# Kernel optimization log

Hardware: AMD Instinct MI355X
Metric: run time of the kernel (lower is better)

Reference implementation:

```python
import jax, jax.numpy as jnp
import numpy as np

N_NODES = 100000
N_EDGES = 1280000
D_IN = 64
D_HID = 64
D_OUT = 1
N_GRAPHS = 512


def setup_inputs() -> dict:
    key = jax.random.key(0)
    ks = jax.random.split(key, 12)
    x = jax.random.normal(ks[0], (N_NODES, D_IN), dtype=jnp.float32)
    edge_index = jax.random.randint(ks[1], (2, N_EDGES), 0, N_NODES, dtype=jnp.int32)
    batch = jnp.sort(jax.random.randint(ks[2], (N_NODES,), 0, N_GRAPHS, dtype=jnp.int32))
    s = 0.1
    w0 = jax.random.normal(ks[3], (D_IN, D_HID), dtype=jnp.float32) * s
    b0 = jnp.zeros((D_HID,), dtype=jnp.float32)
    w1 = jax.random.normal(ks[4], (D_HID, D_HID), dtype=jnp.float32) * s
    b1 = jnp.zeros((D_HID,), dtype=jnp.float32)
    w2 = jax.random.normal(ks[5], (D_HID, D_HID), dtype=jnp.float32) * s
    b2 = jnp.zeros((D_HID,), dtype=jnp.float32)
    fc_w = jax.random.normal(ks[6], (D_HID, D_OUT), dtype=jnp.float32) * s
    fc_b = jnp.zeros((D_OUT,), dtype=jnp.float32)
    return {"x": x, "edge_index": edge_index, "batch": batch,
            "w0": w0, "b0": b0, "w1": w1, "b1": b1, "w2": w2, "b2": b2,
            "fc_w": fc_w, "fc_b": fc_b}


def _gcn_conv(x, w, b, src, dst):
    # PyG GCNConv: h = x @ W; out_i = sum_j norm_ij * h_j over (A + I), sym norm.
    h = x @ w                                           # [N, H]
    ones = jnp.ones((src.shape[0],), dtype=h.dtype)
    deg = jax.ops.segment_sum(ones, dst, num_segments=N_NODES) + 1.0  # +1 self-loop
    dinv = jax.lax.rsqrt(deg)                           # [N]
    norm = dinv[src] * dinv[dst]                        # [E]
    agg = jax.ops.segment_sum(h[src] * norm[:, None], dst, num_segments=N_NODES)
    agg = agg + h * (dinv * dinv)[:, None]              # self-loop term
    return agg + b


def reference(x, edge_index, batch, w0, b0, w1, b1, w2, b2, fc_w, fc_b):
    src, dst = edge_index[0], edge_index[1]
    # 3 stacked GCNConv + relu (dropout is identity in eval mode)
    h = jax.nn.relu(_gcn_conv(x, w0, b0, src, dst))
    h = jax.nn.relu(_gcn_conv(h, w1, b1, src, dst))
    h = jax.nn.relu(_gcn_conv(h, w2, b2, src, dst))
    # global mean pool per graph
    sums = jax.ops.segment_sum(h, batch, num_segments=N_GRAPHS)        # [G, H]
    cnt = jax.ops.segment_sum(jnp.ones((N_NODES,), h.dtype), batch, num_segments=N_GRAPHS)
    mean = sums / jnp.maximum(cnt, 1.0)[:, None]
    return mean @ fc_w + fc_b                            # [G, 1]
```

## Files before the change

kernel.cpp:

```cpp
#include <hip/hip_runtime.h>
#include <hip/hip_fp16.h>
#include <type_traits>

#define N_NODES 100000
#define N_EDGES 1280000
#define N_GRAPHS 512
#define NBK 196
#define CHUNK 3200
#define NCH 400
#define CAP 8192
#define NDCAP 48
#define GEMM_BLOCKS 391

typedef _Float16 v8h __attribute__((ext_vector_type(8)));
typedef float v4f __attribute__((ext_vector_type(4)));

__device__ inline void fmix_lo(float& acc, unsigned h2, float n) {
    asm volatile("v_fma_mix_f32 %0, %1, %2, %0 op_sel:[0,0,0] op_sel_hi:[1,0,0]"
                 : "+v"(acc) : "v"(h2), "v"(n));
}
__device__ inline void fmix_hi(float& acc, unsigned h2, float n) {
    asm volatile("v_fma_mix_f32 %0, %1, %2, %0 op_sel:[1,0,0] op_sel_hi:[1,0,0]"
                 : "+v"(acc) : "v"(h2), "v"(n));
}


template <typename T, bool FOLD>
__device__ inline void gemm_body(int bid, const T* __restrict__ X,
                                 const float* __restrict__ W,
                                 const float* __restrict__ dinv,
                                 __half* __restrict__ H,
                                 _Float16 (*Wt)[72]) {
    int t = threadIdx.x;
    #pragma unroll
    for (int q = 0; q < 4; q++) {
        int idx = t + q * 256;
        int k = idx >> 4;
        int n0 = (idx & 15) * 4;
        float4 v = ((const float4*)W)[idx];
        Wt[n0 + 0][k] = (_Float16)v.x;
        Wt[n0 + 1][k] = (_Float16)v.y;
        Wt[n0 + 2][k] = (_Float16)v.z;
        Wt[n0 + 3][k] = (_Float16)v.w;
    }
    __syncthreads();

    int wv = t >> 6, lane = t & 63;
    int m = lane & 15, quad = lane >> 4;

    v8h bf[4][2];
    #pragma unroll
    for (int c = 0; c < 4; c++)
        #pragma unroll
        for (int h = 0; h < 2; h++)
            bf[c][h] = *(const v8h*)&Wt[c * 16 + m][h * 32 + quad * 8];

    int base = bid * 256 + wv * 64;
    #pragma unroll
    for (int tt = 0; tt < 4; tt++) {
        int tile = base + tt * 16;
        int rA = min(tile + m, N_NODES - 1);
        v8h a0, a1;
        if constexpr (std::is_same<T, float>::value) {
            const float* xp = (const float*)X + (size_t)rA * 64 + quad * 8;
            float4 p0 = *(const float4*)xp;
            float4 p1 = *(const float4*)(xp + 4);
            float4 p2 = *(const float4*)(xp + 32);
            float4 p3 = *(const float4*)(xp + 36);
            a0 = (v8h){(_Float16)p0.x, (_Float16)p0.y, (_Float16)p0.z, (_Float16)p0.w,
                       (_Float16)p1.x, (_Float16)p1.y, (_Float16)p1.z, (_Float16)p1.w};
            a1 = (v8h){(_Float16)p2.x, (_Float16)p2.y, (_Float16)p2.z, (_Float16)p2.w,
                       (_Float16)p3.x, (_Float16)p3.y, (_Float16)p3.z, (_Float16)p3.w};
        } else {
            const _Float16* xp = (const _Float16*)X + (size_t)rA * 64 + quad * 8;
            a0 = *(const v8h*)xp;
            a1 = *(const v8h*)(xp + 32);
        }
        v4f acc[4];
        #pragma unroll
        for (int c = 0; c < 4; c++) {
            acc[c] = (v4f){0.f, 0.f, 0.f, 0.f};
            acc[c] = __builtin_amdgcn_mfma_f32_16x16x32_f16(a0, bf[c][0], acc[c], 0, 0, 0);
            acc[c] = __builtin_amdgcn_mfma_f32_16x16x32_f16(a1, bf[c][1], acc[c], 0, 0, 0);
        }
        #pragma unroll
        for (int r = 0; r < 4; r++) {
            int row = tile + quad * 4 + r;
            if (row < N_NODES) {
                float dv = FOLD ? dinv[row] : 1.0f;
                __half* hp = H + (size_t)row * 64 + m;
                #pragma unroll
                for (int c = 0; c < 4; c++)
                    hp[c * 16] = __float2half(FOLD ? acc[c][r] * dv : acc[c][r]);
            }
        }
    }
}

template <typename T, bool FOLD>
__global__ __launch_bounds__(256) void gemm_mfma(const T* __restrict__ X,
                                                 const float* __restrict__ W,
                                                 const float* __restrict__ dinv,
                                                 __half* __restrict__ H) {
    __shared__ _Float16 Wt[64][72];
    gemm_body<T, FOLD>(blockIdx.x, X, W, dinv, H, Wt);
}


#define SC_BUF   0
#define SC_LCNT  (CHUNK * 4)
#define SC_LLOC  (SC_LCNT + NBK * 4)
#define SC_LCUR  (SC_LLOC + NBK * 4)
#define SC_S     (SC_LCUR + NBK * 4)
#define SC_BYTES (SC_S + 256 * 4)

__global__ __launch_bounds__(256) void scatter_gemm(const int* __restrict__ src,
                                                    const int* __restrict__ dst,
                                                    int* __restrict__ bcur,
                                                    unsigned* __restrict__ pairs,
                                                    const float* __restrict__ x,
                                                    const float* __restrict__ w0,
                                                    __half* __restrict__ H) {
    alignas(16) __shared__ char smem[SC_BYTES];
    if (blockIdx.x >= NCH) {
        gemm_body<float, false>(blockIdx.x - NCH, x, w0, nullptr, H,
                                (_Float16(*)[72])smem);
        return;
    }
    unsigned* buf  = (unsigned*)(smem + SC_BUF);
    int*      lcnt = (int*)(smem + SC_LCNT);
    int*      lloc = (int*)(smem + SC_LLOC);
    int*      lcur = (int*)(smem + SC_LCUR);
    int*      s    = (int*)(smem + SC_S);
    int t = threadIdx.x;
    for (int k = t; k < NBK; k += 256) { lcnt[k] = 0; lcur[k] = 0; }
    __syncthreads();
    int e0 = blockIdx.x * CHUNK;
    for (int i = t; i < CHUNK; i += 256) atomicAdd(&lcnt[dst[e0 + i] >> 9], 1);
    __syncthreads();
    {
        int v = (t < NBK) ? lcnt[t] : 0;
        s[t] = v; __syncthreads();
        for (int d = 1; d < 256; d <<= 1) {
            int xx = (t >= d) ? s[t - d] : 0;
            __syncthreads();
            s[t] += xx;
            __syncthreads();
        }
        if (t < NBK) lloc[t] = s[t] - v;
    }
    __syncthreads();
    for (int i = t; i < CHUNK; i += 256) {
        int d = dst[e0 + i];
        int k = d >> 9;
        int li = lloc[k] + atomicAdd(&lcur[k], 1);
        buf[li] = ((unsigned)src[e0 + i] << 9) | (unsigned)(d & 511);
    }
    __syncthreads();
    for (int k = t; k < NBK; k += 256) {
        int c = lcnt[k];
        if (c) {
            int g = atomicAdd(&bcur[k * 16], c);
            int lo = lloc[k];
            unsigned* dstp = pairs + (size_t)k * CAP;
            for (int j = 0; j < c; j++)
                if (g + j < CAP) dstp[g + j] = buf[lo + j];
        }
    }
}


__global__ __launch_bounds__(256) void bucket_place(const unsigned* __restrict__ pairs,
                                                    const int* __restrict__ bcur,
                                                    uint2* __restrict__ meta,
                                                    float* __restrict__ dinv,
                                                    int* __restrict__ csr) {
    __shared__ int lcur[256];
    __shared__ int lsrc[256 * NDCAP];
    int t = threadIdx.x;
    int bb = blockIdx.x;
    int b = bb >> 1, half = bb & 1;
    int node0 = bb << 8;
    int cnt = min(bcur[b * 16], CAP);
    lcur[t] = 0;
    for (int j = t; j < 256 * NDCAP; j += 256) lsrc[j] = N_NODES;
    __syncthreads();
    const unsigned* prs = pairs + (size_t)b * CAP;
    for (int i = t; i < cnt; i += 256) {
        unsigned pr = prs[i];
        int n = pr & 511;
        if ((n >> 8) == half) {
            int li = atomicAdd(&lcur[n & 255], 1);
            if (li < NDCAP) lsrc[(n & 255) * NDCAP + li] = (int)(pr >> 9);
        }
    }
    __syncthreads();
    int node = node0 + t;
    if (node < N_NODES) {
        int deg = min(lcur[t], NDCAP);
        int degp = (deg + 15) & ~15;
        float dv = 1.0f / sqrtf((float)deg + 1.0f);
        dinv[node] = dv;
        uint2 m;
        m.x = __float_as_uint(dv);
        m.y = (unsigned)degp;
        meta[node] = m;
    }
    const int4* ls4 = (const int4*)lsrc;
    int4* cs4 = (int4*)(csr + (size_t)node0 * NDCAP);
    for (int j = t; j < 256 * NDCAP / 4; j += 256) cs4[j] = ls4[j];
    if (bb == 0 && t == 0) dinv[N_NODES] = 0.f;
}


template <bool FULL>
__device__ inline void chunk_acc2(const char* __restrict__ Hb,
                                  const float* __restrict__ dinv,
                                  unsigned fqo, int4 cA, int4 cB,
                                  float4& a0A, float4& a1A,
                                  float4& a0B, float4& a1B) {
    uint2 uA0 = *(const uint2*)(Hb + (((unsigned)cA.x << 7) | fqo));
    uint2 uA1 = *(const uint2*)(Hb + (((unsigned)cA.y << 7) | fqo));
    uint2 uA2 = *(const uint2*)(Hb + (((unsigned)cA.z << 7) | fqo));
    uint2 uA3 = *(const uint2*)(Hb + (((unsigned)cA.w << 7) | fqo));
    uint2 uB0 = *(const uint2*)(Hb + (((unsigned)cB.x << 7) | fqo));
    uint2 uB1 = *(const uint2*)(Hb + (((unsigned)cB.y << 7) | fqo));
    uint2 uB2 = *(const uint2*)(Hb + (((unsigned)cB.z << 7) | fqo));
    uint2 uB3 = *(const uint2*)(Hb + (((unsigned)cB.w << 7) | fqo));
    float nA0 = FULL ? dinv[cA.x] : 1.0f;
    float nA1 = FULL ? dinv[cA.y] : 1.0f;
    float nA2 = FULL ? dinv[cA.z] : 1.0f;
    float nA3 = FULL ? dinv[cA.w] : 1.0f;
    float nB0 = FULL ? dinv[cB.x] : 1.0f;
    float nB1 = FULL ? dinv[cB.y] : 1.0f;
    float nB2 = FULL ? dinv[cB.z] : 1.0f;
    float nB3 = FULL ? dinv[cB.w] : 1.0f;
    fmix_lo(a0A.x, uA0.x, nA0); fmix_hi(a0A.y, uA0.x, nA0);
    fmix_lo(a0A.z, uA0.y, nA0); fmix_hi(a0A.w, uA0.y, nA0);
    fmix_lo(a1A.x, uA1.x, nA1); fmix_hi(a1A.y, uA1.x, nA1);
    fmix_lo(a1A.z, uA1.y, nA1); fmix_hi(a1A.w, uA1.y, nA1);
    fmix_lo(a0A.x, uA2.x, nA2); fmix_hi(a0A.y, uA2.x, nA2);
    fmix_lo(a0A.z, uA2.y, nA2); fmix_hi(a0A.w, uA2.y, nA2);
    fmix_lo(a1A.x, uA3.x, nA3); fmix_hi(a1A.y, uA3.x, nA3);
    fmix_lo(a1A.z, uA3.y, nA3); fmix_hi(a1A.w, uA3.y, nA3);
    fmix_lo(a0B.x, uB0.x, nB0); fmix_hi(a0B.y, uB0.x, nB0);
    fmix_lo(a0B.z, uB0.y, nB0); fmix_hi(a0B.w, uB0.y, nB0);
    fmix_lo(a1B.x, uB1.x, nB1); fmix_hi(a1B.y, uB1.x, nB1);
    fmix_lo(a1B.z, uB1.y, nB1); fmix_hi(a1B.w, uB1.y, nB1);
    fmix_lo(a0B.x, uB2.x, nB2); fmix_hi(a0B.y, uB2.x, nB2);
    fmix_lo(a0B.z, uB2.y, nB2); fmix_hi(a0B.w, uB2.y, nB2);
    fmix_lo(a1B.x, uB3.x, nB3); fmix_hi(a1B.y, uB3.x, nB3);
    fmix_lo(a1B.z, uB3.y, nB3); fmix_hi(a1B.w, uB3.y, nB3);
}

template <bool FULL>
__device__ inline void agg_pair(const char* __restrict__ Hb, int wid0, int lane,
                                const uint2* __restrict__ meta,
                                const int* __restrict__ csr,
                                const float* __restrict__ dinv,
                                float4& outA, float4& outB) {
    int eg = lane >> 4;
    int fq = lane & 15;
    unsigned fqo = (unsigned)(fq << 3);
    const char* bA = (const char*)(csr + (size_t)wid0 * NDCAP);
    const char* bB = bA + NDCAP * 4;
    int4 cA = *(const int4*)(bA + (eg << 4));
    int4 cB = *(const int4*)(bB + (eg << 4));
    int4 mm = *(const int4*)(meta + wid0);
    float diA = __int_as_float(mm.x);
    int degpA = mm.y;
    float diB = __int_as_float(mm.z);
    int degpB = mm.w;
    uint2 usA = *(const uint2*)(Hb + (((unsigned)wid0 << 7) | fqo));
    uint2 usB = *(const uint2*)(Hb + (((unsigned)(wid0 + 1) << 7) | fqo));

    float4 a0A = {0.f, 0.f, 0.f, 0.f}, a1A = {0.f, 0.f, 0.f, 0.f};
    float4 a0B = {0.f, 0.f, 0.f, 0.f}, a1B = {0.f, 0.f, 0.f, 0.f};
    chunk_acc2<FULL>(Hb, dinv, fqo, cA, cB, a0A, a1A, a0B, a1B);
    int dmax = max(degpA, degpB);
    for (int c = 16; c < dmax; c += 16) {
        int4 tA = *(const int4*)(bA + (c << 2) + (eg << 4));
        int4 tB = *(const int4*)(bB + (c << 2) + (eg << 4));
        chunk_acc2<FULL>(Hb, dinv, fqo, tA, tB, a0A, a1A, a0B, a1B);
    }
    a0A.x += a1A.x; a0A.y += a1A.y; a0A.z += a1A.z; a0A.w += a1A.w;
    a0B.x += a1B.x; a0B.y += a1B.y; a0B.z += a1B.z; a0B.w += a1B.w;
    a0A.x += __shfl_xor(a0A.x, 16); a0A.y += __shfl_xor(a0A.y, 16);
    a0A.z += __shfl_xor(a0A.z, 16); a0A.w += __shfl_xor(a0A.w, 16);
    a0A.x += __shfl_xor(a0A.x, 32); a0A.y += __shfl_xor(a0A.y, 32);
    a0A.z += __shfl_xor(a0A.z, 32); a0A.w += __shfl_xor(a0A.w, 32);
    a0B.x += __shfl_xor(a0B.x, 16); a0B.y += __shfl_xor(a0B.y, 16);
    a0B.z += __shfl_xor(a0B.z, 16); a0B.w += __shfl_xor(a0B.w, 16);
    a0B.x += __shfl_xor(a0B.x, 32); a0B.y += __shfl_xor(a0B.y, 32);
    a0B.z += __shfl_xor(a0B.z, 32); a0B.w += __shfl_xor(a0B.w, 32);
    float2 sA01 = __half22float2(*(__half2*)&usA.x);
    float2 sA23 = __half22float2(*(__half2*)&usA.y);
    float2 sB01 = __half22float2(*(__half2*)&usB.x);
    float2 sB23 = __half22float2(*(__half2*)&usB.y);
    float swA = FULL ? diA : 1.0f;
    float swB = FULL ? diB : 1.0f;
    outA.x = (a0A.x + sA01.x * swA) * diA;
    outA.y = (a0A.y + sA01.y * swA) * diA;
    outA.z = (a0A.z + sA23.x * swA) * diA;
    outA.w = (a0A.w + sA23.y * swA) * diA;
    outB.x = (a0B.x + sB01.x * swB) * diB;
    outB.y = (a0B.y + sB01.y * swB) * diB;
    outB.z = (a0B.z + sB23.x * swB) * diB;
    outB.w = (a0B.w + sB23.y * swB) * diB;
}

template <bool FULL>
__global__ __launch_bounds__(256) void agg_gcn(const __half* __restrict__ H,
                                               const uint2* __restrict__ meta,
                                               const int* __restrict__ csr,
                                               const float* __restrict__ dinv,
                                               const float* __restrict__ bias,
                                               __half* __restrict__ Out) {
    int wid0 = ((blockIdx.x * 256 + threadIdx.x) >> 6) * 2;
    int lane = threadIdx.x & 63;
    if (wid0 >= N_NODES) return;
    float4 rA, rB;
    agg_pair<FULL>((const char*)H, wid0, lane, meta, csr, dinv, rA, rB);
    int fq = lane & 15;
    int eg = lane >> 4;
    if (eg < 2) {
        float4 r;
        r.x = eg ? rB.x : rA.x;
        r.y = eg ? rB.y : rA.y;
        r.z = eg ? rB.z : rA.z;
        r.w = eg ? rB.w : rA.w;
        float4 b4 = ((const float4*)bias)[fq];
        __half2 h01 = __float22half2_rn(make_float2(fmaxf(r.x + b4.x, 0.f),
                                                    fmaxf(r.y + b4.y, 0.f)));
        __half2 h23 = __float22half2_rn(make_float2(fmaxf(r.z + b4.z, 0.f),
                                                    fmaxf(r.w + b4.w, 0.f)));
        uint2 u;
        u.x = *(unsigned int*)&h01;
        u.y = *(unsigned int*)&h23;
        ((uint2*)Out)[(size_t)(wid0 + eg) * 16 + fq] = u;
    }
}

__global__ __launch_bounds__(256) void agg_gcn_pool(const __half* __restrict__ H,
                                                    const uint2* __restrict__ meta,
                                                    const int* __restrict__ csr,
                                                    const float* __restrict__ dinv,
                                                    const float* __restrict__ bias,
                                                    const float* __restrict__ fcw,
                                                    float* __restrict__ p) {
    int wid0 = ((blockIdx.x * 256 + threadIdx.x) >> 6) * 2;
    int lane = threadIdx.x & 63;
    if (wid0 >= N_NODES) return;
    float4 rA, rB;
    agg_pair<false>((const char*)H, wid0, lane, meta, csr, dinv, rA, rB);
    int fq = lane & 15;
    float4 b4 = ((const float4*)bias)[fq];
    float4 f4 = ((const float4*)fcw)[fq];
    float vA = fmaxf(rA.x + b4.x, 0.f) * f4.x + fmaxf(rA.y + b4.y, 0.f) * f4.y
             + fmaxf(rA.z + b4.z, 0.f) * f4.z + fmaxf(rA.w + b4.w, 0.f) * f4.w;
    float vB = fmaxf(rB.x + b4.x, 0.f) * f4.x + fmaxf(rB.y + b4.y, 0.f) * f4.y
             + fmaxf(rB.z + b4.z, 0.f) * f4.z + fmaxf(rB.w + b4.w, 0.f) * f4.w;
    vA += __shfl_xor(vA, 1); vA += __shfl_xor(vA, 2);
    vA += __shfl_xor(vA, 4); vA += __shfl_xor(vA, 8);
    vB += __shfl_xor(vB, 1); vB += __shfl_xor(vB, 2);
    vB += __shfl_xor(vB, 4); vB += __shfl_xor(vB, 8);
    if (lane == 0) {
        p[wid0] = vA;
        p[wid0 + 1] = vB;
    }
}


__device__ inline int lower_bound_batch(const int* __restrict__ batch, int key) {
    int lo = 0, hi = N_NODES;
    while (lo < hi) {
        int mid = (lo + hi) >> 1;
        if (batch[mid] < key) lo = mid + 1; else hi = mid;
    }
    return lo;
}

__global__ __launch_bounds__(256) void graph_reduce(const float* __restrict__ p,
                                                    const int* __restrict__ batch,
                                                    const float* __restrict__ fcb,
                                                    float* __restrict__ out) {
    __shared__ float red[4];
    int g = blockIdx.x;
    int s0 = lower_bound_batch(batch, g);
    int s1 = lower_bound_batch(batch, g + 1);
    float acc = 0.f;
    for (int i = s0 + threadIdx.x; i < s1; i += 256) acc += p[i];
    #pragma unroll
    for (int o = 32; o > 0; o >>= 1) acc += __shfl_xor(acc, o);
    int lane = threadIdx.x & 63, wv = threadIdx.x >> 6;
    if (lane == 0) red[wv] = acc;
    __syncthreads();
    if (threadIdx.x == 0) {
        float sum = red[0] + red[1] + red[2] + red[3];
        out[g] = sum / fmaxf((float)(s1 - s0), 1.f) + fcb[0];
    }
}


extern "C" void kernel_launch(void* const* d_in, const int* in_sizes, int n_in,
                              void* d_out, int out_size, void* d_ws, size_t ws_size,
                              hipStream_t stream) {
    const float* x    = (const float*)d_in[0];
    const int*   ei   = (const int*)d_in[1];
    const int*   batch= (const int*)d_in[2];
    const float* w0   = (const float*)d_in[3];
    const float* b0   = (const float*)d_in[4];
    const float* w1   = (const float*)d_in[5];
    const float* b1   = (const float*)d_in[6];
    const float* w2   = (const float*)d_in[7];
    const float* b2   = (const float*)d_in[8];
    const float* fcw  = (const float*)d_in[9];
    const float* fcb  = (const float*)d_in[10];
    float* out = (float*)d_out;

    const int* src_e = ei;
    const int* dst_e = ei + N_EDGES;

    char* w = (char*)d_ws;
    size_t o = 0;
    int*      bcur = (int*)(w + o);      o += 256 * 16 * 4;
    uint2*    meta = (uint2*)(w + o);    o += (size_t)(N_NODES + 8) * 8;
    float*    dinv = (float*)(w + o);    o += (size_t)(N_NODES + 8) * 4;
    unsigned* pairs= (unsigned*)(w + o); o += (size_t)NBK * CAP * 4;
    int*      csr  = (int*)(w + o);      o += (size_t)(2 * NBK * 256) * NDCAP * 4;
    __half*   bufA = (__half*)(w + o);   o += (size_t)(N_NODES + 1) * 64 * 2;
    __half*   bufB = (__half*)(w + o);   o += (size_t)N_NODES * 64 * 2;
    float*    pvec = (float*)(w + o);    o += (size_t)N_NODES * 4;

    hipMemsetAsync(bcur, 0, 256 * 16 * 4, stream);
    hipMemsetAsync(bufA + (size_t)N_NODES * 64, 0, 128, stream);

    const int AGG_BLOCKS = N_NODES / 8;

    scatter_gemm<<<NCH + GEMM_BLOCKS, 256, 0, stream>>>(src_e, dst_e, bcur, pairs,
                                                        x, w0, bufA);
    bucket_place<<<2 * NBK, 256, 0, stream>>>(pairs, bcur, meta, dinv, csr);

    agg_gcn<true><<<AGG_BLOCKS, 256, 0, stream>>>(bufA, meta, csr, dinv, b0, bufB);

    gemm_mfma<__half, true><<<GEMM_BLOCKS, 256, 0, stream>>>(bufB, w1, dinv, bufA);
    agg_gcn<false><<<AGG_BLOCKS, 256, 0, stream>>>(bufA, meta, csr, dinv, b1, bufB);

    gemm_mfma<__half, true><<<GEMM_BLOCKS, 256, 0, stream>>>(bufB, w2, dinv, bufA);
    agg_gcn_pool<<<AGG_BLOCKS, 256, 0, stream>>>(bufA, meta, csr, dinv, b2, fcw, pvec);

    graph_reduce<<<N_GRAPHS, 256, 0, stream>>>(pvec, batch, fcb, out);
}
```

Measured before the change: 286.0 us.

## Fold self-loop into CSR neighbor list and write only used CSR chunks

Each node's own index is inserted as the first entry of its CSR row, so the self-loop term is aggregated by the normal gather loop instead of a separate load and combine. bucket_place also computes per-pair chunk counts and writes only the CSR chunks the aggregation will read, which cuts global write traffic. The self-loop slot takes one of the NDCAP entries, which lowers the effective neighbor cap. For FULL, the self term is now weighted through the dinv lookup in chunk_acc2, so correctness depends on how that path handles FULL versus non-FULL.

```diff
diff --git a/kernel.cpp b/kernel.cpp
--- a/kernel.cpp
+++ b/kernel.cpp
@@ -11,6 +11,7 @@
 #define CAP 8192
 #define NDCAP 48
 #define GEMM_BLOCKS 391
+#define AGG_BLOCKS 12500
 
 typedef _Float16 v8h __attribute__((ext_vector_type(8)));
 typedef float v4f __attribute__((ext_vector_type(4)));
@@ -176,15 +177,17 @@
                                                     float* __restrict__ dinv,
                                                     int* __restrict__ csr) {
     __shared__ int lcur[256];
+    __shared__ int dmaxc[128];
     __shared__ int lsrc[256 * NDCAP];
     int t = threadIdx.x;
     int bb = blockIdx.x;
     int b = bb >> 1, half = bb & 1;
     int node0 = bb << 8;
     int cnt = min(bcur[b * 16], CAP);
-    lcur[t] = 0;
+    lcur[t] = 1;
     for (int j = t; j < 256 * NDCAP; j += 256) lsrc[j] = N_NODES;
     __syncthreads();
+    lsrc[t * NDCAP] = (node0 + t < N_NODES) ? (node0 + t) : N_NODES;
     const unsigned* prs = pairs + (size_t)b * CAP;
     for (int i = t; i < cnt; i += 256) {
         unsigned pr = prs[i];
@@ -196,9 +199,10 @@
     }
     __syncthreads();
     int node = node0 + t;
+    int tot = min(lcur[t], NDCAP);
     if (node < N_NODES) {
-        int deg = min(lcur[t], NDCAP);
-        int degp = (deg + 15) & ~15;
+        int deg = tot - 1;
+        int degp = (tot + 15) & ~15;
         float dv = 1.0f / sqrtf((float)deg + 1.0f);
         dinv[node] = dv;
         uint2 m;
@@ -206,9 +210,20 @@
         m.y = (unsigned)degp;
         meta[node] = m;
     }
+    if (t < 128) {
+        int t0 = min(lcur[2 * t], NDCAP);
+        int t1 = min(lcur[2 * t + 1], NDCAP);
+        int c0 = (t0 + 15) >> 4, c1 = (t1 + 15) >> 4;
+        dmaxc[t] = max(c0, c1);
+    }
+    __syncthreads();
     const int4* ls4 = (const int4*)lsrc;
     int4* cs4 = (int4*)(csr + (size_t)node0 * NDCAP);
-    for (int j = t; j < 256 * NDCAP / 4; j += 256) cs4[j] = ls4[j];
+    for (int j = t; j < 256 * (NDCAP / 4); j += 256) {
+        int nl = j / (NDCAP / 4);
+        int i4 = j - nl * (NDCAP / 4);
+        if ((i4 >> 2) < dmaxc[nl >> 1]) cs4[j] = ls4[j];
+    }
     if (bb == 0 && t == 0) dinv[N_NODES] = 0.f;
 }
 
@@ -268,16 +283,12 @@
     int4 cB = *(const int4*)(bB + (eg << 4));
     int4 mm = *(const int4*)(meta + wid0);
     float diA = __int_as_float(mm.x);
-    int degpA = mm.y;
     float diB = __int_as_float(mm.z);
-    int degpB = mm.w;
-    uint2 usA = *(const uint2*)(Hb + (((unsigned)wid0 << 7) | fqo));
-    uint2 usB = *(const uint2*)(Hb + (((unsigned)(wid0 + 1) << 7) | fqo));
+    int dmax = max(mm.y, mm.w);
 
     float4 a0A = {0.f, 0.f, 0.f, 0.f}, a1A = {0.f, 0.f, 0.f, 0.f};
     float4 a0B = {0.f, 0.f, 0.f, 0.f}, a1B = {0.f, 0.f, 0.f, 0.f};
     chunk_acc2<FULL>(Hb, dinv, fqo, cA, cB, a0A, a1A, a0B, a1B);
-    int dmax = max(degpA, degpB);
     for (int c = 16; c < dmax; c += 16) {
         int4 tA = *(const int4*)(bA + (c << 2) + (eg << 4));
         int4 tB = *(const int4*)(bB + (c << 2) + (eg << 4));
@@ -293,20 +304,10 @@
     a0B.z += __shfl_xor(a0B.z, 16); a0B.w += __shfl_xor(a0B.w, 16);
     a0B.x += __shfl_xor(a0B.x, 32); a0B.y += __shfl_xor(a0B.y, 32);
     a0B.z += __shfl_xor(a0B.z, 32); a0B.w += __shfl_xor(a0B.w, 32);
-    float2 sA01 = __half22float2(*(__half2*)&usA.x);
-    float2 sA23 = __half22float2(*(__half2*)&usA.y);
-    float2 sB01 = __half22float2(*(__half2*)&usB.x);
-    float2 sB23 = __half22float2(*(__half2*)&usB.y);
-    float swA = FULL ? diA : 1.0f;
-    float swB = FULL ? diB : 1.0f;
-    outA.x = (a0A.x + sA01.x * swA) * diA;
-    outA.y = (a0A.y + sA01.y * swA) * diA;
-    outA.z = (a0A.z + sA23.x * swA) * diA;
-    outA.w = (a0A.w + sA23.y * swA) * diA;
-    outB.x = (a0B.x + sB01.x * swB) * diB;
-    outB.y = (a0B.y + sB01.y * swB) * diB;
-    outB.z = (a0B.z + sB23.x * swB) * diB;
-    outB.w = (a0B.w + sB23.y * swB) * diB;
+    outA.x = a0A.x * diA; outA.y = a0A.y * diA;
+    outA.z = a0A.z * diA; outA.w = a0A.w * diA;
+    outB.x = a0B.x * diB; outB.y = a0B.y * diB;
+    outB.z = a0B.z * diB; outB.w = a0B.w * diB;
 }
 
 template <bool FULL>
@@ -435,8 +436,6 @@
     hipMemsetAsync(bcur, 0, 256 * 16 * 4, stream);
     hipMemsetAsync(bufA + (size_t)N_NODES * 64, 0, 128, stream);
 
-    const int AGG_BLOCKS = N_NODES / 8;
-
     scatter_gemm<<<NCH + GEMM_BLOCKS, 256, 0, stream>>>(src_e, dst_e, bcur, pairs,
                                                         x, w0, bufA);
     bucket_place<<<2 * NBK, 256, 0, stream>>>(pairs, bcur, meta, dinv, csr);
```

Measured after the change: 286.6 us. No clear change (+0.2%).
